# Performance work log

Measured on AMD Instinct MI355X. Metric: run time of the kernel, lower is better.

Reference implementation:

```python
import jax, jax.numpy as jnp
import numpy as np
from jax import lax

T, K, D = 2097152, 8, 4
LOG_2PI = float(np.log(2.0 * np.pi))


def setup_inputs() -> dict:
    key = jax.random.key(0)
    k1, k2, k3, k4 = jax.random.split(key, 4)
    return {
        "x_seq": jax.random.normal(k1, (T, D), dtype=jnp.float32),
        "unnormalized_trans": jax.random.normal(k2, (K, K), dtype=jnp.float32),
        "unnormalized_pi": jax.random.normal(k3, (K,), dtype=jnp.float32),
        "means": jax.random.normal(k4, (K, D), dtype=jnp.float32) * 0.01,
        "log_std": jnp.zeros((K, D), dtype=jnp.float32),
    }


def reference(x_seq, unnormalized_trans, unnormalized_pi, means, log_std):
    # Row-stochastic transition / initial distributions in log space
    log_trans = jax.nn.log_softmax(unnormalized_trans, axis=-1)  # [K, K]
    log_pi = jax.nn.log_softmax(unnormalized_pi, axis=-1)        # [K]

    # Diagonal-Gaussian log emission densities: [T, K]
    std = jnp.exp(log_std)                                        # [K, D]
    z = (x_seq[:, None, :] - means[None, :, :]) / std[None, :, :]  # [T, K, D]
    log_em = jnp.sum(-0.5 * LOG_2PI - log_std[None] - 0.5 * z * z, axis=-1)  # [T, K]

    # Forward algorithm in log space (strictly sequential recurrence)
    alpha0 = log_pi + log_em[0]  # [K]

    def step(alpha, em_t):
        # alpha[i] + log_trans[i, j], logsumexp over source state i
        alpha = em_t + jax.scipy.special.logsumexp(alpha[:, None] + log_trans, axis=0)
        return alpha, None

    alpha, _ = lax.scan(step, alpha0, log_em[1:])
    return jax.scipy.special.logsumexp(alpha, axis=0)
```

## Files before the change

### kernel.cpp

```cpp
#include <hip/hip_runtime.h>
#include <math.h>

#define T_LEN 2097152
#define K 8
#define D 4
#define CHUNK 8
#define TPB 256
#define NBLK (T_LEN / (CHUNK * TPB))
#define MSTRIDE 65

typedef float f2 __attribute__((ext_vector_type(2)));

__device__ __forceinline__ f2 fma2(f2 a, f2 b, f2 c) { return __builtin_elementwise_fma(a, b, c); }
__device__ __forceinline__ f2 max2(f2 a, f2 b) { return __builtin_elementwise_max(a, b); }
__device__ __forceinline__ f2 splat(float s) { f2 r; r.x = s; r.y = s; return r; }


__device__ __forceinline__ void renorm_matf(float P[K][K], float& shift) {
    float mx = 0.f;
#pragma unroll
    for (int i = 0; i < K; ++i)
#pragma unroll
        for (int j = 0; j < K; ++j) mx = fmaxf(mx, P[i][j]);
    int ex = (__float_as_int(mx) >> 23) & 255;
    float scale = __int_as_float((254 - ex) << 23);
    shift += (float)(ex - 127);
#pragma unroll
    for (int i = 0; i < K; ++i)
#pragma unroll
        for (int j = 0; j < K; ++j) P[i][j] *= scale;
}

__device__ __forceinline__ void mat_combine(const float L[K][K], const float R[K][K], float C[K][K]) {
#pragma unroll
    for (int i = 0; i < K; ++i) {
        float q[K];
#pragma unroll
        for (int j = 0; j < K; ++j) q[j] = L[i][0] * R[0][j];
#pragma unroll
        for (int k = 1; k < K; ++k)
#pragma unroll
            for (int j = 0; j < K; ++j) q[j] = fmaf(L[i][k], R[k][j], q[j]);
#pragma unroll
        for (int j = 0; j < K; ++j) C[i][j] = q[j];
    }
}

__device__ __forceinline__ void combine_stream(const float* __restrict__ Lp,
                                               const float* __restrict__ Rp,
                                               float C[K][K]) {
#pragma unroll
    for (int k = 0; k < K; ++k) {
        float Lc[K], Rr[K];
#pragma unroll
        for (int i = 0; i < K; ++i) Lc[i] = Lp[i * 8 + k];
#pragma unroll
        for (int j = 0; j < K; ++j) Rr[j] = Rp[k * 8 + j];
        if (k == 0) {
#pragma unroll
            for (int i = 0; i < K; ++i)
#pragma unroll
                for (int j = 0; j < K; ++j) C[i][j] = Lc[i] * Rr[j];
        } else {
#pragma unroll
            for (int i = 0; i < K; ++i)
#pragma unroll
                for (int j = 0; j < K; ++j) C[i][j] = fmaf(Lc[i], Rr[j], C[i][j]);
        }
    }
}

__device__ __forceinline__ void tree_levels(float* lm, float* lsh) {
    const int g = threadIdx.x >> 3;
    const int i = threadIdx.x & 7;
#pragma unroll 1
    for (int lvl = 1; lvl <= 7; ++lvl) {
        const int c = 64 >> (lvl - 1);
        const int S = 1 << (lvl - 1);
#pragma unroll 1
        for (int m = g; m < c; m += 32) {
            const int li = 2 * m * S, ri = li + S;
            const float* Lp = lm + li * MSTRIDE;
            const float* Rp = lm + ri * MSTRIDE;
            float Lr[8];
#pragma unroll
            for (int k = 0; k < 8; ++k) Lr[k] = Lp[i * 8 + k];
            float q[8];
#pragma unroll
            for (int j = 0; j < 8; ++j) q[j] = Lr[0] * Rp[j];
#pragma unroll
            for (int k = 1; k < 8; ++k)
#pragma unroll
                for (int j = 0; j < 8; ++j) q[j] = fmaf(Lr[k], Rp[k * 8 + j], q[j]);
            float mx = fmaxf(fmaxf(fmaxf(q[0], q[1]), fmaxf(q[2], q[3])),
                             fmaxf(fmaxf(q[4], q[5]), fmaxf(q[6], q[7])));
            mx = fmaxf(mx, __shfl_xor(mx, 1));
            mx = fmaxf(mx, __shfl_xor(mx, 2));
            mx = fmaxf(mx, __shfl_xor(mx, 4));
            int ex = (__float_as_int(mx) >> 23) & 255;
            float scale = __int_as_float((254 - ex) << 23);
            float ns = lsh[li] + lsh[ri] + (float)(ex - 127);
            float* Op = lm + li * MSTRIDE + i * 8;
#pragma unroll
            for (int j = 0; j < 8; ++j) Op[j] = q[j] * scale;
            if (i == 0) lsh[li] = ns;
        }
        __syncthreads();
    }
}

__device__ __forceinline__ void hybrid_tree(float P[K][K], float& shift, float* lm, float* lsh) {
    const int t = threadIdx.x;
    if ((t & 1) == 0) {
#pragma unroll
        for (int i = 0; i < K; ++i)
#pragma unroll
            for (int j = 0; j < K; ++j) lm[(t >> 1) * MSTRIDE + i * 8 + j] = P[i][j];
        lsh[t >> 1] = shift;
    }
    __syncthreads();
    if (t & 1) {
        float L[K][K];
#pragma unroll
        for (int i = 0; i < K; ++i)
#pragma unroll
            for (int k = 0; k < K; ++k) L[i][k] = lm[(t >> 1) * MSTRIDE + i * 8 + k];
        float C[K][K];
        mat_combine(L, P, C);
        float ns = shift + lsh[t >> 1];
        renorm_matf(C, ns);
#pragma unroll
        for (int i = 0; i < K; ++i)
#pragma unroll
            for (int j = 0; j < K; ++j) lm[(t >> 1) * MSTRIDE + i * 8 + j] = C[i][j];
        lsh[t >> 1] = ns;
    }
    __syncthreads();
    tree_levels(lm, lsh);
}

__device__ __forceinline__ float emit_e2(const f2 ca2[4], const f2 cb2[4][4],
                                         const f2 cc2[4][4], float4 x, f2 e2[4]) {
    f2 x0 = splat(x.x), x1 = splat(x.y), x2 = splat(x.z), x3 = splat(x.w);
    f2 em2[4];
#pragma unroll
    for (int jj = 0; jj < 4; ++jj) {
        f2 t = ca2[jj];
        t = fma2(fma2(cc2[0][jj], x0, cb2[0][jj]), x0, t);
        t = fma2(fma2(cc2[1][jj], x1, cb2[1][jj]), x1, t);
        t = fma2(fma2(cc2[2][jj], x2, cb2[2][jj]), x2, t);
        t = fma2(fma2(cc2[3][jj], x3, cb2[3][jj]), x3, t);
        em2[jj] = t;
    }
    f2 m2 = max2(max2(em2[0], em2[1]), max2(em2[2], em2[3]));
    float me = fmaxf(m2.x, m2.y);
#pragma unroll
    for (int jj = 0; jj < 4; ++jj) {
        e2[jj].x = exp2f(em2[jj].x - me);
        e2[jj].y = exp2f(em2[jj].y - me);
    }
    return me;
}

__global__ void hmm_setup(const float* __restrict__ x,
                          const float* __restrict__ ut,
                          const float* __restrict__ up,
                          const float* __restrict__ mn,
                          const float* __restrict__ lsd,
                          float* __restrict__ ws) {
    const int lane = threadIdx.x;
    const float L2PI = 1.83787706640934548356f;
    const float LOG2E = 1.44269504088896340736f;

    float v = ut[lane];
    float m = v;
    m = fmaxf(m, __shfl_xor(m, 1));
    m = fmaxf(m, __shfl_xor(m, 2));
    m = fmaxf(m, __shfl_xor(m, 4));
    float e = expf(v - m);
    float s = e;
    s += __shfl_xor(s, 1); s += __shfl_xor(s, 2); s += __shfl_xor(s, 4);
    ws[lane] = e / s;

    float pv = up[lane & 7];
    float pm = pv;
    pm = fmaxf(pm, __shfl_xor(pm, 1));
    pm = fmaxf(pm, __shfl_xor(pm, 2));
    pm = fmaxf(pm, __shfl_xor(pm, 4));
    float pe = expf(pv - pm);
    float ps = pe;
    ps += __shfl_xor(ps, 1); ps += __shfl_xor(ps, 2); ps += __shfl_xor(ps, 4);
    float pival = pe / ps;

    int k = (lane & 31) >> 2, d = lane & 3;
    float lv = lsd[k * D + d];
    float mu = mn[k * D + d];
    float iv = expf(-2.f * lv);
    float bn = mu * iv;
    float cn = -0.5f * iv;
    float aterm = -0.5f * L2PI - lv - 0.5f * mu * mu * iv;
    float ak = aterm;
    ak += __shfl_xor(ak, 1); ak += __shfl_xor(ak, 2);
    if (lane < 32) {
        ws[72 + lane]  = bn * LOG2E;
        ws[104 + lane] = cn * LOG2E;
        if (d == 0) ws[64 + k] = ak * LOG2E;
    }

    float xd = x[d];
    float part = (cn * xd + bn) * xd + aterm;
    part += __shfl_xor(part, 1); part += __shfl_xor(part, 2);
    float pik = __shfl(pival, k);
    if (lane < 32 && d == 0) ws[136 + k] = pik * expf(part);
}

__global__ __launch_bounds__(TPB) void hmm_main(const float* __restrict__ x,
                                                const float* __restrict__ cst,
                                                float* __restrict__ bp,
                                                float* __restrict__ bs) {
    __shared__ float lm[128 * MSTRIDE];
    __shared__ float lsh[128];
    const int tid = blockIdx.x * TPB + threadIdx.x;

    float Tr[K][K];
#pragma unroll
    for (int i = 0; i < K; ++i)
#pragma unroll
        for (int j = 0; j < K; ++j) Tr[i][j] = cst[i * K + j];
    f2 Tr2[K][4];
#pragma unroll
    for (int i = 0; i < K; ++i)
#pragma unroll
        for (int jj = 0; jj < 4; ++jj) { Tr2[i][jj].x = Tr[i][2 * jj]; Tr2[i][jj].y = Tr[i][2 * jj + 1]; }

    f2 ca2[4], cb2[4][4], cc2[4][4];
#pragma unroll
    for (int jj = 0; jj < 4; ++jj) {
        ca2[jj].x = cst[64 + 2 * jj]; ca2[jj].y = cst[64 + 2 * jj + 1];
#pragma unroll
        for (int d = 0; d < 4; ++d) {
            cb2[d][jj].x = cst[72 + (2 * jj) * 4 + d];  cb2[d][jj].y = cst[72 + (2 * jj + 1) * 4 + d];
            cc2[d][jj].x = cst[104 + (2 * jj) * 4 + d]; cc2[d][jj].y = cst[104 + (2 * jj + 1) * 4 + d];
        }
    }

    const float4* xv = reinterpret_cast<const float4*>(x) + (size_t)tid * CHUNK;
    float4 xr[CHUNK];
#pragma unroll
    for (int t = 0; t < CHUNK; ++t) xr[t] = xv[t];

    f2 T2[K][4];
    float shift;
    {
        f2 eB[4];
        float meB = emit_e2(ca2, cb2, cc2, xr[1], eB);
        if (tid == 0) {
#pragma unroll
            for (int i = 0; i < K; ++i) {
                f2 a0 = splat(cst[136 + i]);
#pragma unroll
                for (int jj = 0; jj < 4; ++jj) T2[i][jj] = a0 * Tr2[i][jj] * eB[jj];
            }
            shift = meB;
        } else {
            f2 eA[4];
            float meA = emit_e2(ca2, cb2, cc2, xr[0], eA);
#pragma unroll
            for (int i = 0; i < K; ++i) {
                f2 ei = splat((i & 1) ? eA[i >> 1].y : eA[i >> 1].x);
#pragma unroll
                for (int jj = 0; jj < 4; ++jj) T2[i][jj] = ei * Tr2[i][jj] * eB[jj];
            }
            shift = meA + meB;
        }
    }

#pragma unroll
    for (int p = 1; p < 4; ++p) {
        f2 eA[4], eB[4];
        float meA = emit_e2(ca2, cb2, cc2, xr[2 * p], eA);
        float meB = emit_e2(ca2, cb2, cc2, xr[2 * p + 1], eB);
        shift += meA + meB;
#pragma unroll
        for (int i = 0; i < K; ++i) {
            f2 r2[4];
#pragma unroll
            for (int kk = 0; kk < 4; ++kk) r2[kk] = T2[i][kk] * eA[kk];
            f2 u[4];
#pragma unroll
            for (int jj = 0; jj < 4; ++jj) u[jj] = splat(r2[0].x) * Tr2[0][jj];
#pragma unroll
            for (int k = 1; k < 8; ++k) {
                f2 rk = splat((k & 1) ? r2[k >> 1].y : r2[k >> 1].x);
#pragma unroll
                for (int jj = 0; jj < 4; ++jj) u[jj] = fma2(rk, Tr2[k][jj], u[jj]);
            }
#pragma unroll
            for (int jj = 0; jj < 4; ++jj) T2[i][jj] = u[jj] * eB[jj];
        }
    }

    if (tid != 0) {
#pragma unroll
        for (int jj = 0; jj < 4; ++jj) {
            f2 c[K];
#pragma unroll
            for (int k = 0; k < K; ++k) c[k] = T2[k][jj];
#pragma unroll
            for (int i = 0; i < K; ++i) {
                f2 a = splat(Tr[i][0]) * c[0];
#pragma unroll
                for (int k = 1; k < K; ++k) a = fma2(splat(Tr[i][k]), c[k], a);
                T2[i][jj] = a;
            }
        }
    }

    float (*T)[K] = reinterpret_cast<float(*)[K]>(T2);
    renorm_matf(T, shift);

    hybrid_tree(T, shift, lm, lsh);

    if (threadIdx.x == 0) {
        float4* o4 = reinterpret_cast<float4*>(bp + (size_t)blockIdx.x * 64);
        const float4* l4 = reinterpret_cast<const float4*>(lm);
#pragma unroll
        for (int q = 0; q < 16; ++q) o4[q] = l4[q];
        bs[blockIdx.x] = lsh[0];
    }
}

__global__ void hmm_final(const float* __restrict__ bp,
                          const float* __restrict__ bs,
                          float* __restrict__ out) {
    __shared__ float lm[128 * MSTRIDE];
    __shared__ float lsh[128];
    const int t = threadIdx.x;
    const int base = t * 4;

    float P[K][K];
    {
        const float4* p4 = reinterpret_cast<const float4*>(bp + (size_t)base * 64);
        float4* dst = reinterpret_cast<float4*>(&P[0][0]);
#pragma unroll
        for (int q = 0; q < 16; ++q) dst[q] = p4[q];
    }
    float shift = bs[base];
#pragma unroll 1
    for (int r = 1; r < 4; ++r) {
        const float* Rp = bp + (size_t)(base + r) * 64;
        float C[K][K];
        combine_stream(&P[0][0], Rp, C);
        shift += bs[base + r];
        renorm_matf(C, shift);
#pragma unroll
        for (int i = 0; i < K; ++i)
#pragma unroll
            for (int j = 0; j < K; ++j) P[i][j] = C[i][j];
    }

    hybrid_tree(P, shift, lm, lsh);

    if (t == 0) {
        double s = 0.0;
#pragma unroll
        for (int i = 0; i < K; ++i)
#pragma unroll
            for (int j = 0; j < K; ++j) s += (double)lm[i * 8 + j];
        out[0] = (float)(log(s) + (double)lsh[0] * 0.69314718055994530942);
    }
}

extern "C" void kernel_launch(void* const* d_in, const int* in_sizes, int n_in,
                              void* d_out, int out_size, void* d_ws, size_t ws_size,
                              hipStream_t stream) {
    (void)in_sizes; (void)n_in; (void)out_size; (void)ws_size;
    const float* x  = (const float*)d_in[0];
    const float* ut = (const float*)d_in[1];
    const float* up = (const float*)d_in[2];
    const float* mn = (const float*)d_in[3];
    const float* ls = (const float*)d_in[4];
    float* ws  = (float*)d_ws;
    float* out = (float*)d_out;
    float* bp  = ws + 256;
    float* bs  = ws + 256 + (size_t)NBLK * 64;

    hmm_setup<<<1, 64, 0, stream>>>(x, ut, up, mn, ls, ws);
    hmm_main<<<NBLK, TPB, 0, stream>>>(x, ws, bp, bs);
    hmm_final<<<1, TPB, 0, stream>>>(bp, bs, out);
}
```

Measured before the change: 134.8 us.

## Vectorize tree matrix combines with float4 LDS layout and wave-local final levels

```diff
diff --git a/kernel.cpp b/kernel.cpp
--- a/kernel.cpp
+++ b/kernel.cpp
@@ -7,7 +7,7 @@
 #define CHUNK 8
 #define TPB 256
 #define NBLK (T_LEN / (CHUNK * TPB))
-#define MSTRIDE 65
+#define MS4 19
 
 typedef float f2 __attribute__((ext_vector_type(2)));
 
@@ -16,123 +16,136 @@
 __device__ __forceinline__ f2 splat(float s) { f2 r; r.x = s; r.y = s; return r; }
 
 
-__device__ __forceinline__ void renorm_matf(float P[K][K], float& shift) {
-    float mx = 0.f;
-#pragma unroll
-    for (int i = 0; i < K; ++i)
-#pragma unroll
-        for (int j = 0; j < K; ++j) mx = fmaxf(mx, P[i][j]);
+__device__ __forceinline__ float4* matp4(float* lm, int li) {
+    return reinterpret_cast<float4*>(lm) + li * MS4 + ((li >> 1) & 3);
+}
+
+__device__ __forceinline__ void renorm2(f2 M[K][4], float& shift) {
+    f2 m2 = max2(max2(M[0][0], M[0][1]), max2(M[0][2], M[0][3]));
+#pragma unroll
+    for (int i = 1; i < K; ++i)
+        m2 = max2(m2, max2(max2(M[i][0], M[i][1]), max2(M[i][2], M[i][3])));
+    float mx = fmaxf(m2.x, m2.y);
     int ex = (__float_as_int(mx) >> 23) & 255;
     float scale = __int_as_float((254 - ex) << 23);
     shift += (float)(ex - 127);
+    f2 sc = splat(scale);
 #pragma unroll
     for (int i = 0; i < K; ++i)
 #pragma unroll
-        for (int j = 0; j < K; ++j) P[i][j] *= scale;
-}
-
-__device__ __forceinline__ void mat_combine(const float L[K][K], const float R[K][K], float C[K][K]) {
+        for (int jj = 0; jj < 4; ++jj) M[i][jj] = M[i][jj] * sc;
+}
+
+__device__ __forceinline__ void store_mat(float* lm, int li, const f2 M[K][4]) {
+    float4* dst = matp4(lm, li);
 #pragma unroll
     for (int i = 0; i < K; ++i) {
-        float q[K];
-#pragma unroll
-        for (int j = 0; j < K; ++j) q[j] = L[i][0] * R[0][j];
-#pragma unroll
-        for (int k = 1; k < K; ++k)
-#pragma unroll
-            for (int j = 0; j < K; ++j) q[j] = fmaf(L[i][k], R[k][j], q[j]);
-#pragma unroll
-        for (int j = 0; j < K; ++j) C[i][j] = q[j];
-    }
-}
-
-__device__ __forceinline__ void combine_stream(const float* __restrict__ Lp,
-                                               const float* __restrict__ Rp,
-                                               float C[K][K]) {
-#pragma unroll
-    for (int k = 0; k < K; ++k) {
-        float Lc[K], Rr[K];
-#pragma unroll
-        for (int i = 0; i < K; ++i) Lc[i] = Lp[i * 8 + k];
-#pragma unroll
-        for (int j = 0; j < K; ++j) Rr[j] = Rp[k * 8 + j];
+        float4 w0, w1;
+        w0.x = M[i][0].x; w0.y = M[i][0].y; w0.z = M[i][1].x; w0.w = M[i][1].y;
+        w1.x = M[i][2].x; w1.y = M[i][2].y; w1.z = M[i][3].x; w1.w = M[i][3].y;
+        dst[i * 2] = w0;
+        dst[i * 2 + 1] = w1;
+    }
+}
+
+__device__ __forceinline__ void combine8(float* lm, float* lsh, int li, int ri, int i) {
+    const float4* Lb = matp4(lm, li);
+    const float4* Rb = matp4(lm, ri);
+    float4 la = Lb[i * 2], lb = Lb[i * 2 + 1];
+    float4 R[16];
+#pragma unroll
+    for (int q = 0; q < 16; ++q) R[q] = Rb[q];
+    float lk[8] = {la.x, la.y, la.z, la.w, lb.x, lb.y, lb.z, lb.w};
+    f2 acc[4];
+#pragma unroll
+    for (int k = 0; k < 8; ++k) {
+        f2 s = splat(lk[k]);
+        f2 r0, r1, r2_, r3;
+        r0.x = R[2 * k].x;     r0.y = R[2 * k].y;
+        r1.x = R[2 * k].z;     r1.y = R[2 * k].w;
+        r2_.x = R[2 * k + 1].x; r2_.y = R[2 * k + 1].y;
+        r3.x = R[2 * k + 1].z;  r3.y = R[2 * k + 1].w;
         if (k == 0) {
-#pragma unroll
-            for (int i = 0; i < K; ++i)
-#pragma unroll
-                for (int j = 0; j < K; ++j) C[i][j] = Lc[i] * Rr[j];
+            acc[0] = s * r0; acc[1] = s * r1; acc[2] = s * r2_; acc[3] = s * r3;
         } else {
-#pragma unroll
-            for (int i = 0; i < K; ++i)
-#pragma unroll
-                for (int j = 0; j < K; ++j) C[i][j] = fmaf(Lc[i], Rr[j], C[i][j]);
-        }
-    }
+            acc[0] = fma2(s, r0, acc[0]); acc[1] = fma2(s, r1, acc[1]);
+            acc[2] = fma2(s, r2_, acc[2]); acc[3] = fma2(s, r3, acc[3]);
+        }
+    }
+    f2 m2 = max2(max2(acc[0], acc[1]), max2(acc[2], acc[3]));
+    float mx = fmaxf(m2.x, m2.y);
+    mx = fmaxf(mx, __shfl_xor(mx, 1));
+    mx = fmaxf(mx, __shfl_xor(mx, 2));
+    mx = fmaxf(mx, __shfl_xor(mx, 4));
+    int ex = (__float_as_int(mx) >> 23) & 255;
+    float scale = __int_as_float((254 - ex) << 23);
+    float ns = lsh[li] + lsh[ri] + (float)(ex - 127);
+    f2 sc = splat(scale);
+    f2 o0 = acc[0] * sc, o1 = acc[1] * sc, o2 = acc[2] * sc, o3 = acc[3] * sc;
+    float4 w0, w1;
+    w0.x = o0.x; w0.y = o0.y; w0.z = o1.x; w0.w = o1.y;
+    w1.x = o2.x; w1.y = o2.y; w1.z = o3.x; w1.w = o3.y;
+    float4* Ob = matp4(lm, li);
+    Ob[i * 2] = w0;
+    Ob[i * 2 + 1] = w1;
+    if (i == 0) lsh[li] = ns;
 }
 
 __device__ __forceinline__ void tree_levels(float* lm, float* lsh) {
     const int g = threadIdx.x >> 3;
     const int i = threadIdx.x & 7;
 #pragma unroll 1
-    for (int lvl = 1; lvl <= 7; ++lvl) {
+    for (int lvl = 1; lvl <= 3; ++lvl) {
         const int c = 64 >> (lvl - 1);
         const int S = 1 << (lvl - 1);
 #pragma unroll 1
-        for (int m = g; m < c; m += 32) {
-            const int li = 2 * m * S, ri = li + S;
-            const float* Lp = lm + li * MSTRIDE;
-            const float* Rp = lm + ri * MSTRIDE;
-            float Lr[8];
-#pragma unroll
-            for (int k = 0; k < 8; ++k) Lr[k] = Lp[i * 8 + k];
-            float q[8];
-#pragma unroll
-            for (int j = 0; j < 8; ++j) q[j] = Lr[0] * Rp[j];
-#pragma unroll
-            for (int k = 1; k < 8; ++k)
-#pragma unroll
-                for (int j = 0; j < 8; ++j) q[j] = fmaf(Lr[k], Rp[k * 8 + j], q[j]);
-            float mx = fmaxf(fmaxf(fmaxf(q[0], q[1]), fmaxf(q[2], q[3])),
-                             fmaxf(fmaxf(q[4], q[5]), fmaxf(q[6], q[7])));
-            mx = fmaxf(mx, __shfl_xor(mx, 1));
-            mx = fmaxf(mx, __shfl_xor(mx, 2));
-            mx = fmaxf(mx, __shfl_xor(mx, 4));
-            int ex = (__float_as_int(mx) >> 23) & 255;
-            float scale = __int_as_float((254 - ex) << 23);
-            float ns = lsh[li] + lsh[ri] + (float)(ex - 127);
-            float* Op = lm + li * MSTRIDE + i * 8;
-#pragma unroll
-            for (int j = 0; j < 8; ++j) Op[j] = q[j] * scale;
-            if (i == 0) lsh[li] = ns;
-        }
+        for (int m = g; m < c; m += 32) combine8(lm, lsh, 2 * m * S, 2 * m * S + S, i);
         __syncthreads();
     }
-}
-
-__device__ __forceinline__ void hybrid_tree(float P[K][K], float& shift, float* lm, float* lsh) {
+    if (threadIdx.x < 64) {
+#pragma unroll 1
+        for (int lvl = 4; lvl <= 7; ++lvl) {
+            const int c = 64 >> (lvl - 1);
+            const int S = 1 << (lvl - 1);
+            if (g < c) combine8(lm, lsh, 2 * g * S, 2 * g * S + S, i);
+            asm volatile("s_waitcnt lgkmcnt(0)" ::: "memory");
+        }
+    }
+}
+
+__device__ __forceinline__ void hybrid_tree(f2 P2[K][4], float shift, float* lm, float* lsh) {
     const int t = threadIdx.x;
     if ((t & 1) == 0) {
-#pragma unroll
-        for (int i = 0; i < K; ++i)
-#pragma unroll
-            for (int j = 0; j < K; ++j) lm[(t >> 1) * MSTRIDE + i * 8 + j] = P[i][j];
+        store_mat(lm, t >> 1, P2);
         lsh[t >> 1] = shift;
     }
     __syncthreads();
     if (t & 1) {
-        float L[K][K];
-#pragma unroll
-        for (int i = 0; i < K; ++i)
-#pragma unroll
-            for (int k = 0; k < K; ++k) L[i][k] = lm[(t >> 1) * MSTRIDE + i * 8 + k];
-        float C[K][K];
-        mat_combine(L, P, C);
-        float ns = shift + lsh[t >> 1];
-        renorm_matf(C, ns);
-#pragma unroll
-        for (int i = 0; i < K; ++i)
-#pragma unroll
-            for (int j = 0; j < K; ++j) lm[(t >> 1) * MSTRIDE + i * 8 + j] = C[i][j];
+        const float4* src = matp4(lm, t >> 1);
+        float lsv = lsh[t >> 1];
+        f2 C[K][4];
+#pragma unroll
+        for (int i = 0; i < K; ++i) {
+            float4 la = src[i * 2], lb = src[i * 2 + 1];
+            float lk[8] = {la.x, la.y, la.z, la.w, lb.x, lb.y, lb.z, lb.w};
+            f2 q[4];
+#pragma unroll
+            for (int k = 0; k < 8; ++k) {
+                f2 s = splat(lk[k]);
+                if (k == 0) {
+#pragma unroll
+                    for (int jj = 0; jj < 4; ++jj) q[jj] = s * P2[k][jj];
+                } else {
+#pragma unroll
+                    for (int jj = 0; jj < 4; ++jj) q[jj] = fma2(s, P2[k][jj], q[jj]);
+                }
+            }
+#pragma unroll
+            for (int jj = 0; jj < 4; ++jj) C[i][jj] = q[jj];
+        }
+        float ns = shift + lsv;
+        renorm2(C, ns);
+        store_mat(lm, t >> 1, C);
         lsh[t >> 1] = ns;
     }
     __syncthreads();
@@ -218,7 +231,7 @@
                                                 const float* __restrict__ cst,
                                                 float* __restrict__ bp,
                                                 float* __restrict__ bs) {
-    __shared__ float lm[128 * MSTRIDE];
+    __shared__ __align__(16) float lm[128 * 76];
     __shared__ float lsh[128];
     const int tid = blockIdx.x * TPB + threadIdx.x;
 
@@ -316,10 +329,9 @@
         }
     }
 
-    float (*T)[K] = reinterpret_cast<float(*)[K]>(T2);
-    renorm_matf(T, shift);
-
-    hybrid_tree(T, shift, lm, lsh);
+    renorm2(T2, shift);
+
+    hybrid_tree(T2, shift, lm, lsh);
 
     if (threadIdx.x == 0) {
         float4* o4 = reinterpret_cast<float4*>(bp + (size_t)blockIdx.x * 64);
@@ -330,43 +342,70 @@
     }
 }
 
-__global__ void hmm_final(const float* __restrict__ bp,
-                          const float* __restrict__ bs,
-                          float* __restrict__ out) {
-    __shared__ float lm[128 * MSTRIDE];
+__global__ __launch_bounds__(TPB) void hmm_final(const float* __restrict__ bp,
+                                                 const float* __restrict__ bs,
+                                                 float* __restrict__ out) {
+    __shared__ __align__(16) float lm[128 * 76];
     __shared__ float lsh[128];
     const int t = threadIdx.x;
     const int base = t * 4;
 
-    float P[K][K];
+    f2 P2[K][4];
     {
         const float4* p4 = reinterpret_cast<const float4*>(bp + (size_t)base * 64);
-        float4* dst = reinterpret_cast<float4*>(&P[0][0]);
-#pragma unroll
-        for (int q = 0; q < 16; ++q) dst[q] = p4[q];
+#pragma unroll
+        for (int i = 0; i < K; ++i) {
+            float4 a = p4[2 * i], b = p4[2 * i + 1];
+            P2[i][0].x = a.x; P2[i][0].y = a.y;
+            P2[i][1].x = a.z; P2[i][1].y = a.w;
+            P2[i][2].x = b.x; P2[i][2].y = b.y;
+            P2[i][3].x = b.z; P2[i][3].y = b.w;
+        }
     }
     float shift = bs[base];
 #pragma unroll 1
     for (int r = 1; r < 4; ++r) {
-        const float* Rp = bp + (size_t)(base + r) * 64;
-        float C[K][K];
-        combine_stream(&P[0][0], Rp, C);
+        const float4* r4 = reinterpret_cast<const float4*>(bp + (size_t)(base + r) * 64);
+        float4 R[16];
+#pragma unroll
+        for (int q = 0; q < 16; ++q) R[q] = r4[q];
+        f2 C[K][4];
+#pragma unroll
+        for (int i = 0; i < K; ++i) {
+            f2 q[4];
+#pragma unroll
+            for (int k = 0; k < 8; ++k) {
+                float pk_ = (k & 1) ? P2[i][k >> 1].y : P2[i][k >> 1].x;
+                f2 s = splat(pk_);
+                f2 r0, r1, r2_, r3;
+                r0.x = R[2 * k].x;      r0.y = R[2 * k].y;
+                r1.x = R[2 * k].z;      r1.y = R[2 * k].w;
+                r2_.x = R[2 * k + 1].x; r2_.y = R[2 * k + 1].y;
+                r3.x = R[2 * k + 1].z;  r3.y = R[2 * k + 1].w;
+                if (k == 0) {
+                    q[0] = s * r0; q[1] = s * r1; q[2] = s * r2_; q[3] = s * r3;
+                } else {
+                    q[0] = fma2(s, r0, q[0]); q[1] = fma2(s, r1, q[1]);
+                    q[2] = fma2(s, r2_, q[2]); q[3] = fma2(s, r3, q[3]);
+                }
+            }
+#pragma unroll
+            for (int jj = 0; jj < 4; ++jj) C[i][jj] = q[jj];
+        }
         shift += bs[base + r];
-        renorm_matf(C, shift);
+        renorm2(C, shift);
 #pragma unroll
         for (int i = 0; i < K; ++i)
 #pragma unroll
-            for (int j = 0; j < K; ++j) P[i][j] = C[i][j];
-    }
-
-    hybrid_tree(P, shift, lm, lsh);
+            for (int jj = 0; jj < 4; ++jj) P2[i][jj] = C[i][jj];
+    }
+
+    hybrid_tree(P2, shift, lm, lsh);
 
     if (t == 0) {
         double s = 0.0;
 #pragma unroll
-        for (int i = 0; i < K; ++i)
-#pragma unroll
-            for (int j = 0; j < K; ++j) s += (double)lm[i * 8 + j];
+        for (int i = 0; i < 64; ++i) s += (double)lm[i];
         out[0] = (float)(log(s) + (double)lsh[0] * 0.69314718055994530942);
     }
 }
```

Measured after the change: 124.5 us. 7.6% less time.
